# Performance work log

Hardware: AMD Instinct MI355X
Metric: run time of the kernel (lower is better)

The kernel has to match this reference:

```python
import jax, jax.numpy as jnp
import numpy as np

V, E, H = 50000, 512, 1024
HD = H // 2            # per-direction LSTM hidden
T = 2048               # sequence length
TAGS, START, STOP = 32, 30, 31
NEG = -10000.0


def setup_inputs() -> dict:
    key = jax.random.key(0)
    ks = jax.random.split(key, 14)
    s = 1.0 / np.sqrt(HD)
    u = lambda k, shape: jax.random.uniform(k, shape, jnp.float32, -s, s)
    sentence = jax.random.randint(ks[0], (T,), 0, V)
    emb = jax.random.normal(ks[1], (V, E), jnp.float32)
    # PyTorch LSTM gate layout: [i, f, g, o] stacked along dim 0
    w_ih_f, w_hh_f, b_f = u(ks[2], (4 * HD, E)), u(ks[3], (4 * HD, HD)), u(ks[4], (4 * HD,))
    w_ih_b, w_hh_b, b_b = u(ks[5], (4 * HD, E)), u(ks[6], (4 * HD, HD)), u(ks[7], (4 * HD,))
    W_out = u(ks[8], (TAGS, H))
    b_out = u(ks[9], (TAGS,))
    transitions = jax.random.normal(ks[10], (TAGS, TAGS), jnp.float32)
    transitions = transitions.at[START, :].set(NEG).at[:, STOP].set(NEG)
    h0 = jax.random.normal(ks[11], (2, HD), jnp.float32)  # [dir, HD], batch=1 squeezed
    c0 = jax.random.normal(ks[12], (2, HD), jnp.float32)
    return dict(sentence=sentence, emb=emb, w_ih_f=w_ih_f, w_hh_f=w_hh_f, b_f=b_f,
                w_ih_b=w_ih_b, w_hh_b=w_hh_b, b_b=b_b, W_out=W_out, b_out=b_out,
                transitions=transitions, h0=h0, c0=c0)


def _lstm_dir(x, h0, c0, w_ih, w_hh, b, reverse):
    # x: [T, E]; single-sequence LSTM scan, gates ordered i,f,g,o as in torch
    xg = x @ w_ih.T + b  # [T, 4*HD], precompute input contribution
    def step(carry, xt):
        h, c = carry
        g = xt + w_hh @ h
        i, f, gg, o = jnp.split(g, 4)
        c = jax.nn.sigmoid(f) * c + jax.nn.sigmoid(i) * jnp.tanh(gg)
        h = jax.nn.sigmoid(o) * jnp.tanh(c)
        return (h, c), h
    _, hs = jax.lax.scan(step, (h0, c0), xg, reverse=reverse)
    return hs  # [T, HD]


def _viterbi(feats, transitions):
    # feats: [T, TAGS]
    init = jnp.full((TAGS,), NEG, feats.dtype).at[START].set(0.0)
    def step(fv, feat):
        scores = fv[None, :] + transitions       # [next, prev]
        bp = jnp.argmax(scores, axis=1)          # [TAGS]
        fv_new = jnp.max(scores, axis=1) + feat
        return fv_new, bp
    fv, bps = jax.lax.scan(step, init, feats)
    terminal = fv + transitions[STOP]
    best = jnp.argmax(terminal)
    score = terminal[best]
    def back(tag, bp):
        return bp[tag], tag
    _, path = jax.lax.scan(back, best, bps, reverse=True)
    return score, path  # path: [T] int tags


def reference(sentence, emb, w_ih_f, w_hh_f, b_f, w_ih_b, w_hh_b, b_b,
              W_out, b_out, transitions, h0, c0):
    x = emb[sentence]  # [T, E]
    hf = _lstm_dir(x, h0[0], c0[0], w_ih_f, w_hh_f, b_f, reverse=False)
    hb = _lstm_dir(x, h0[1], c0[1], w_ih_b, w_hh_b, b_b, reverse=True)
    feats = jnp.concatenate([hf, hb], axis=-1) @ W_out.T + b_out  # [T, TAGS]
    score, path = _viterbi(feats, transitions)
    return score, path
```

## Files before the change

### kernel.cpp

```cpp
#include <hip/hip_runtime.h>
#include <math.h>

#define TT 2048
#define EE 512
#define HDD 512
#define TAGS 32
#define STARTT 30
#define STOPP 31
#define NEGV -10000.0f
#define VCH 256
#define SENT 0xFFFFFFFFu

__global__ __launch_bounds__(256) void k_xgemm(const int* __restrict__ sent,
        const float* __restrict__ emb,
        const float* __restrict__ wf, const float* __restrict__ wb,
        const float* __restrict__ bf, const float* __restrict__ bb,
        float* __restrict__ xg, int* __restrict__ xflag) {
    const int jj   = blockIdx.y >> 1;
    const int dir  = blockIdx.y & 1;
    const int tile = dir ? (31 - jj) : jj;
    const float* __restrict__ w    = dir ? wb : wf;
    const float* __restrict__ bias = dir ? bb : bf;
    const int tb = tile * 64;
    const int nb = blockIdx.x * 64;
    __shared__ float As[64][17];
    __shared__ float Bs[64][17];
    const int tid = threadIdx.x;
    const int lr = tid >> 2;
    const int lc = (tid & 3) * 4;
    const int ty = tid >> 4;
    const int tx = tid & 15;
    const int sidx = sent[tb + lr];
    float acc[4][4] = {};
    for (int k0 = 0; k0 < EE; k0 += 16) {
        float4 av = *(const float4*)(emb + (size_t)sidx * EE + k0 + lc);
        float4 bv = *(const float4*)(w + (size_t)(nb + lr) * EE + k0 + lc);
        As[lr][lc+0] = av.x; As[lr][lc+1] = av.y; As[lr][lc+2] = av.z; As[lr][lc+3] = av.w;
        Bs[lr][lc+0] = bv.x; Bs[lr][lc+1] = bv.y; Bs[lr][lc+2] = bv.z; Bs[lr][lc+3] = bv.w;
        __syncthreads();
        #pragma unroll
        for (int kk = 0; kk < 16; ++kk) {
            float a[4], b[4];
            #pragma unroll
            for (int i = 0; i < 4; ++i) a[i] = As[ty*4+i][kk];
            #pragma unroll
            for (int j = 0; j < 4; ++j) b[j] = Bs[tx*4+j][kk];
            #pragma unroll
            for (int i = 0; i < 4; ++i)
                #pragma unroll
                for (int j = 0; j < 4; ++j)
                    acc[i][j] += a[i] * b[j];
        }
        __syncthreads();
    }
    #pragma unroll
    for (int i = 0; i < 4; ++i) {
        float4 o;
        o.x = acc[i][0] + bias[nb + tx*4 + 0];
        o.y = acc[i][1] + bias[nb + tx*4 + 1];
        o.z = acc[i][2] + bias[nb + tx*4 + 2];
        o.w = acc[i][3] + bias[nb + tx*4 + 3];
        *(float4*)(xg + ((size_t)dir*TT + tb + ty*4 + i) * 2048 + nb + tx*4) = o;
    }
    __syncthreads();
    if (tid == 0)
        __hip_atomic_fetch_add(&xflag[dir * 32 + tile], 1,
                               __ATOMIC_RELEASE, __HIP_MEMORY_SCOPE_AGENT);
}

__device__ __forceinline__ float fsig(float x) {
    return __builtin_amdgcn_rcpf(1.f + __expf(-x));
}
__device__ __forceinline__ float ftanh(float x) {
    return 2.f * __builtin_amdgcn_rcpf(1.f + __expf(-2.f * x)) - 1.f;
}

__device__ __forceinline__ void waitflag(const int* f) {
    while (__hip_atomic_load(f, __ATOMIC_ACQUIRE, __HIP_MEMORY_SCOPE_AGENT) < 32)
        __builtin_amdgcn_s_sleep(1);
}

__global__ __launch_bounds__(256, 1) void k_lstm(const float* __restrict__ xg,
        const float* __restrict__ whhf, const float* __restrict__ whhb,
        const float* __restrict__ h0, const float* __restrict__ c0,
        float* __restrict__ hs, const int* __restrict__ xflag) {
    const int dir = blockIdx.y;
    const float* __restrict__ whh = dir ? whhb : whhf;
    const int tid    = threadIdx.x;
    const int lane   = tid & 63;
    const int waveid = tid >> 6;
    const int unit   = lane >> 4;
    const int gate   = (lane >> 2) & 3;
    const int seg    = lane & 3;
    const int ubase  = (blockIdx.x * 4 + waveid) * 4;
    const int grow   = gate * HDD + ubase + unit;

    float4 w[32];
    {
        const float4* wp = (const float4*)(whh + (size_t)grow * HDD + seg * 128);
        #pragma unroll
        for (int i = 0; i < 32; ++i) w[i] = wp[i];
    }

    __shared__ float hbuf[2][528];

    float c = c0[dir * HDD + ubase + unit];

    const int* flags = xflag + dir * 32;
    const int t0 = dir ? (TT - 1) : 0;
    int curtile = t0 >> 6;
    waitflag(&flags[curtile]);
    float xvn = __uint_as_float(__hip_atomic_load(
        (const unsigned*)(xg + ((size_t)dir * TT + t0) * 2048 + grow),
        __ATOMIC_RELAXED, __HIP_MEMORY_SCOPE_AGENT));

    const int g0 = 2 * tid;
    const int soff = (g0 >> 7) * 132 + (g0 & 127);
    hbuf[0][soff]     = h0[dir * HDD + g0];
    hbuf[0][soff + 1] = h0[dir * HDD + g0 + 1];

    for (int s = 0; s < TT; ++s) {
        const int t = dir ? (TT - 1 - s) : s;
        const float xv = xvn;
        if (s + 1 < TT) {
            const int tn = dir ? (TT - 2 - s) : (s + 1);
            const int tilen = tn >> 6;
            if (tilen != curtile) { waitflag(&flags[tilen]); curtile = tilen; }
            xvn = __uint_as_float(__hip_atomic_load(
                (const unsigned*)(xg + ((size_t)dir * TT + tn) * 2048 + grow),
                __ATOMIC_RELAXED, __HIP_MEMORY_SCOPE_AGENT));
        }

        float* hb = hbuf[s & 1];
        if (s > 0) {
            const int tprev = dir ? (t + 1) : (t - 1);
            const unsigned long long* hsrc = (const unsigned long long*)
                (hs + ((size_t)dir * TT + tprev) * HDD) + tid;
            unsigned long long vv = __hip_atomic_load(hsrc,
                    __ATOMIC_RELAXED, __HIP_MEMORY_SCOPE_AGENT);
            while ((unsigned)vv == SENT || (unsigned)(vv >> 32) == SENT)
                vv = __hip_atomic_load(hsrc,
                        __ATOMIC_RELAXED, __HIP_MEMORY_SCOPE_AGENT);
            hb[soff]     = __uint_as_float((unsigned)vv);
            hb[soff + 1] = __uint_as_float((unsigned)(vv >> 32));
        }
        __syncthreads();

        const float4* hp = (const float4*)(hb + seg * 132);
        float a0 = 0.f, a1 = 0.f, a2 = 0.f, a3 = 0.f;
        #pragma unroll
        for (int i = 0; i < 32; i += 4) {
            float4 h0v = hp[i], h1v = hp[i+1], h2v = hp[i+2], h3v = hp[i+3];
            a0 += w[i  ].x*h0v.x + w[i  ].y*h0v.y + w[i  ].z*h0v.z + w[i  ].w*h0v.w;
            a1 += w[i+1].x*h1v.x + w[i+1].y*h1v.y + w[i+1].z*h1v.z + w[i+1].w*h1v.w;
            a2 += w[i+2].x*h2v.x + w[i+2].y*h2v.y + w[i+2].z*h2v.z + w[i+2].w*h2v.w;
            a3 += w[i+3].x*h3v.x + w[i+3].y*h3v.y + w[i+3].z*h3v.z + w[i+3].w*h3v.w;
        }
        float acc = (a0 + a1) + (a2 + a3);
        acc += __shfl_xor(acc, 1);
        acc += __shfl_xor(acc, 2);
        acc += xv;

        const int base = lane & ~15;
        const float iv = __shfl(acc, base + 0);
        const float fv = __shfl(acc, base + 4);
        const float gv = __shfl(acc, base + 8);
        const float ov = __shfl(acc, base + 12);
        c = fsig(fv) * c + fsig(iv) * ftanh(gv);
        const float h = fsig(ov) * ftanh(c);

        if ((lane & 15) == 0)
            __hip_atomic_store(&hs[((size_t)dir * TT + t) * HDD + ubase + unit], h,
                               __ATOMIC_RELAXED, __HIP_MEMORY_SCOPE_AGENT);
    }
}

__global__ __launch_bounds__(256) void k_feats(const float* __restrict__ hs,
        const float* __restrict__ Wout, const float* __restrict__ bout,
        float* __restrict__ feats) {
    const int t = blockIdx.x;
    const int tid = threadIdx.x;
    const int tag = tid >> 3;
    const int chunk = tid & 7;
    const float* __restrict__ hrow = (chunk < 4)
        ? hs + (size_t)t * HDD
        : hs + ((size_t)TT + t) * HDD - 512;
    float acc = 0.f;
    const float4* wp = (const float4*)(Wout + (size_t)tag * 1024 + chunk * 128);
    const float4* hp = (const float4*)(hrow + chunk * 128);
    #pragma unroll
    for (int i = 0; i < 32; ++i) {
        float4 wv = wp[i];
        float4 hv = hp[i];
        acc += wv.x*hv.x + wv.y*hv.y + wv.z*hv.z + wv.w*hv.w;
    }
    __shared__ float red[TAGS][9];
    red[tag][chunk] = acc;
    __syncthreads();
    if (tid < TAGS) {
        float s = bout[tid];
        #pragma unroll
        for (int c = 0; c < 8; ++c) s += red[tid][c];
        feats[(size_t)t * TAGS + tid] = s;
    }
}

__global__ __launch_bounds__(64) void k_viterbi(const float* __restrict__ feats,
        const float* __restrict__ trans, float* __restrict__ out) {
    const int lane = threadIdx.x;
    const int n  = lane & 31;
    const int ph = lane >> 5;
    __shared__ float fvs[TAGS];
    __shared__ unsigned char bp[TT][TAGS];
    __shared__ __align__(16) float fbuf[VCH * TAGS];
    float tr[16];
    #pragma unroll
    for (int p = 0; p < 16; ++p) tr[p] = trans[n * TAGS + ph * 16 + p];
    if (lane < TAGS) fvs[lane] = (lane == STARTT) ? 0.f : NEGV;
    __syncthreads();
    for (int c0 = 0; c0 < TT; c0 += VCH) {
        const float4* src = (const float4*)(feats + (size_t)c0 * TAGS);
        float4* dst = (float4*)fbuf;
        for (int i = lane; i < VCH * TAGS / 4; i += 64) dst[i] = src[i];
        __syncthreads();
        for (int lt = 0; lt < VCH; ++lt) {
            const int t = c0 + lt;
            float bv = fvs[ph * 16] + tr[0];
            int bi = ph * 16;
            #pragma unroll
            for (int p = 1; p < 16; ++p) {
                const float cand = fvs[ph * 16 + p] + tr[p];
                if (cand > bv) { bv = cand; bi = ph * 16 + p; }
            }
            const float obv = __shfl_xor(bv, 32);
            const int   obi = __shfl_xor(bi, 32);
            if (obv > bv || (obv == bv && obi < bi)) { bv = obv; bi = obi; }
            const float nf = bv + fbuf[lt * TAGS + n];
            if (ph == 0) bp[t][n] = (unsigned char)bi;
            __syncthreads();
            if (ph == 0) fvs[n] = nf;
            __syncthreads();
        }
    }
    if (lane < TAGS) fvs[lane] += trans[STOPP * TAGS + lane];
    __syncthreads();
    if (lane == 0) {
        float bs = fvs[0]; int best = 0;
        for (int i = 1; i < TAGS; ++i)
            if (fvs[i] > bs) { bs = fvs[i]; best = i; }
        out[0] = bs;
        int tag = best;
        for (int t = TT - 1; t >= 0; --t) {
            out[1 + t] = (float)tag;
            tag = bp[t][tag];
        }
    }
}

extern "C" void kernel_launch(void* const* d_in, const int* in_sizes, int n_in,
                              void* d_out, int out_size, void* d_ws, size_t ws_size,
                              hipStream_t stream) {
    const int*   sent  = (const int*)  d_in[0];
    const float* emb   = (const float*)d_in[1];
    const float* wihf  = (const float*)d_in[2];
    const float* whhf  = (const float*)d_in[3];
    const float* bfv   = (const float*)d_in[4];
    const float* wihb  = (const float*)d_in[5];
    const float* whhb  = (const float*)d_in[6];
    const float* bbv   = (const float*)d_in[7];
    const float* Wout  = (const float*)d_in[8];
    const float* bout  = (const float*)d_in[9];
    const float* trans = (const float*)d_in[10];
    const float* h0    = (const float*)d_in[11];
    const float* c0    = (const float*)d_in[12];
    float* out = (float*)d_out;

    char* ws = (char*)d_ws;
    float* xg    = (float*)(ws + ((size_t)4  << 20));
    float* hs    = (float*)(ws + ((size_t)36 << 20));
    float* feats = (float*)(ws + ((size_t)44 << 20));
    int* xflag   = (int*)  (ws + ((size_t)44 << 20) + (320u << 10));

    hipMemsetAsync(hs, 0xFF, (size_t)2 * TT * HDD * sizeof(float), stream);
    hipMemsetAsync(xflag, 0, 64 * sizeof(int), stream);
    k_xgemm  <<<dim3(32, 64), 256, 0, stream>>>(sent, emb, wihf, wihb, bfv, bbv,
                                                xg, xflag);
    k_lstm   <<<dim3(32, 2), 256, 0, stream>>>(xg, whhf, whhb, h0, c0, hs, xflag);
    k_feats  <<<TT, 256, 0, stream>>>(hs, Wout, bout, feats);
    k_viterbi<<<1, 64, 0, stream>>>(feats, trans, out);
}
```

Before: 4.496 ms.

## Interleave forward and backward LSTM directions within each block to hide sync latency

The LSTM kernel now runs both directions in the same 32 blocks instead of 64 blocks split by direction. Each block holds both recurrent weight slices in registers and alternates a backward step and a forward step, so the cross-block polling for one direction overlaps with compute for the other. This halves the number of blocks participating in each spin-wait and doubles the register footprint (256 floats of weights per thread), which risks spilling or lower clocks. The serial chain per block also becomes twice as long per iteration.

```diff
diff --git a/kernel.cpp b/kernel.cpp
--- a/kernel.cpp
+++ b/kernel.cpp
@@ -84,8 +84,6 @@
         const float* __restrict__ whhf, const float* __restrict__ whhb,
         const float* __restrict__ h0, const float* __restrict__ c0,
         float* __restrict__ hs, const int* __restrict__ xflag) {
-    const int dir = blockIdx.y;
-    const float* __restrict__ whh = dir ? whhb : whhf;
     const int tid    = threadIdx.x;
     const int lane   = tid & 63;
     const int waveid = tid >> 6;
@@ -95,83 +93,134 @@
     const int ubase  = (blockIdx.x * 4 + waveid) * 4;
     const int grow   = gate * HDD + ubase + unit;
 
-    float4 w[32];
+    float4 wF[32], wB[32];
     {
-        const float4* wp = (const float4*)(whh + (size_t)grow * HDD + seg * 128);
+        const float4* wp = (const float4*)(whhf + (size_t)grow * HDD + seg * 128);
         #pragma unroll
-        for (int i = 0; i < 32; ++i) w[i] = wp[i];
-    }
-
-    __shared__ float hbuf[2][528];
-
-    float c = c0[dir * HDD + ubase + unit];
-
-    const int* flags = xflag + dir * 32;
-    const int t0 = dir ? (TT - 1) : 0;
-    int curtile = t0 >> 6;
-    waitflag(&flags[curtile]);
-    float xvn = __uint_as_float(__hip_atomic_load(
-        (const unsigned*)(xg + ((size_t)dir * TT + t0) * 2048 + grow),
-        __ATOMIC_RELAXED, __HIP_MEMORY_SCOPE_AGENT));
+        for (int i = 0; i < 32; ++i) wF[i] = wp[i];
+        const float4* wq = (const float4*)(whhb + (size_t)grow * HDD + seg * 128);
+        #pragma unroll
+        for (int i = 0; i < 32; ++i) wB[i] = wq[i];
+    }
+
+    __shared__ float hbF[528];
+    __shared__ float hbB[528];
+
+    float cF = c0[ubase + unit];
+    float cB = c0[HDD + ubase + unit];
 
     const int g0 = 2 * tid;
     const int soff = (g0 >> 7) * 132 + (g0 & 127);
-    hbuf[0][soff]     = h0[dir * HDD + g0];
-    hbuf[0][soff + 1] = h0[dir * HDD + g0 + 1];
+    hbF[soff]     = h0[g0];
+    hbF[soff + 1] = h0[g0 + 1];
+    hbB[soff]     = h0[HDD + g0];
+    hbB[soff + 1] = h0[HDD + g0 + 1];
+
+    const int* flagsF = xflag;
+    const int* flagsB = xflag + 32;
+    int ctF = 0, ctB = 31;
+    waitflag(&flagsF[0]);
+    waitflag(&flagsB[31]);
+    float xvF = __uint_as_float(__hip_atomic_load(
+        (const unsigned*)(xg + (size_t)0 * 2048 + grow),
+        __ATOMIC_RELAXED, __HIP_MEMORY_SCOPE_AGENT));
+    float xvB = __uint_as_float(__hip_atomic_load(
+        (const unsigned*)(xg + ((size_t)TT + TT - 1) * 2048 + grow),
+        __ATOMIC_RELAXED, __HIP_MEMORY_SCOPE_AGENT));
 
     for (int s = 0; s < TT; ++s) {
-        const int t = dir ? (TT - 1 - s) : s;
-        const float xv = xvn;
+        const int tf = s;
+        const int tb = TT - 1 - s;
+        const float xf = xvF, xb = xvB;
         if (s + 1 < TT) {
-            const int tn = dir ? (TT - 2 - s) : (s + 1);
-            const int tilen = tn >> 6;
-            if (tilen != curtile) { waitflag(&flags[tilen]); curtile = tilen; }
-            xvn = __uint_as_float(__hip_atomic_load(
-                (const unsigned*)(xg + ((size_t)dir * TT + tn) * 2048 + grow),
+            const int tfn = s + 1, tbn = TT - 2 - s;
+            if ((tfn >> 6) != ctF) { waitflag(&flagsF[tfn >> 6]); ctF = tfn >> 6; }
+            if ((tbn >> 6) != ctB) { waitflag(&flagsB[tbn >> 6]); ctB = tbn >> 6; }
+            xvF = __uint_as_float(__hip_atomic_load(
+                (const unsigned*)(xg + (size_t)tfn * 2048 + grow),
                 __ATOMIC_RELAXED, __HIP_MEMORY_SCOPE_AGENT));
-        }
-
-        float* hb = hbuf[s & 1];
+            xvB = __uint_as_float(__hip_atomic_load(
+                (const unsigned*)(xg + ((size_t)TT + tbn) * 2048 + grow),
+                __ATOMIC_RELAXED, __HIP_MEMORY_SCOPE_AGENT));
+        }
+
         if (s > 0) {
-            const int tprev = dir ? (t + 1) : (t - 1);
             const unsigned long long* hsrc = (const unsigned long long*)
-                (hs + ((size_t)dir * TT + tprev) * HDD) + tid;
+                (hs + ((size_t)TT + tb + 1) * HDD) + tid;
             unsigned long long vv = __hip_atomic_load(hsrc,
                     __ATOMIC_RELAXED, __HIP_MEMORY_SCOPE_AGENT);
             while ((unsigned)vv == SENT || (unsigned)(vv >> 32) == SENT)
                 vv = __hip_atomic_load(hsrc,
                         __ATOMIC_RELAXED, __HIP_MEMORY_SCOPE_AGENT);
-            hb[soff]     = __uint_as_float((unsigned)vv);
-            hb[soff + 1] = __uint_as_float((unsigned)(vv >> 32));
-        }
-        __syncthreads();
-
-        const float4* hp = (const float4*)(hb + seg * 132);
-        float a0 = 0.f, a1 = 0.f, a2 = 0.f, a3 = 0.f;
-        #pragma unroll
-        for (int i = 0; i < 32; i += 4) {
-            float4 h0v = hp[i], h1v = hp[i+1], h2v = hp[i+2], h3v = hp[i+3];
-            a0 += w[i  ].x*h0v.x + w[i  ].y*h0v.y + w[i  ].z*h0v.z + w[i  ].w*h0v.w;
-            a1 += w[i+1].x*h1v.x + w[i+1].y*h1v.y + w[i+1].z*h1v.z + w[i+1].w*h1v.w;
-            a2 += w[i+2].x*h2v.x + w[i+2].y*h2v.y + w[i+2].z*h2v.z + w[i+2].w*h2v.w;
-            a3 += w[i+3].x*h3v.x + w[i+3].y*h3v.y + w[i+3].z*h3v.z + w[i+3].w*h3v.w;
-        }
-        float acc = (a0 + a1) + (a2 + a3);
-        acc += __shfl_xor(acc, 1);
-        acc += __shfl_xor(acc, 2);
-        acc += xv;
-
-        const int base = lane & ~15;
-        const float iv = __shfl(acc, base + 0);
-        const float fv = __shfl(acc, base + 4);
-        const float gv = __shfl(acc, base + 8);
-        const float ov = __shfl(acc, base + 12);
-        c = fsig(fv) * c + fsig(iv) * ftanh(gv);
-        const float h = fsig(ov) * ftanh(c);
-
-        if ((lane & 15) == 0)
-            __hip_atomic_store(&hs[((size_t)dir * TT + t) * HDD + ubase + unit], h,
-                               __ATOMIC_RELAXED, __HIP_MEMORY_SCOPE_AGENT);
+            hbB[soff]     = __uint_as_float((unsigned)vv);
+            hbB[soff + 1] = __uint_as_float((unsigned)(vv >> 32));
+        }
+        __syncthreads();
+        {
+            const float4* hp = (const float4*)(hbB + seg * 132);
+            float a0 = 0.f, a1 = 0.f, a2 = 0.f, a3 = 0.f;
+            #pragma unroll
+            for (int i = 0; i < 32; i += 4) {
+                float4 h0v = hp[i], h1v = hp[i+1], h2v = hp[i+2], h3v = hp[i+3];
+                a0 += wB[i  ].x*h0v.x + wB[i  ].y*h0v.y + wB[i  ].z*h0v.z + wB[i  ].w*h0v.w;
+                a1 += wB[i+1].x*h1v.x + wB[i+1].y*h1v.y + wB[i+1].z*h1v.z + wB[i+1].w*h1v.w;
+                a2 += wB[i+2].x*h2v.x + wB[i+2].y*h2v.y + wB[i+2].z*h2v.z + wB[i+2].w*h2v.w;
+                a3 += wB[i+3].x*h3v.x + wB[i+3].y*h3v.y + wB[i+3].z*h3v.z + wB[i+3].w*h3v.w;
+            }
+            float acc = (a0 + a1) + (a2 + a3);
+            acc += __shfl_xor(acc, 1);
+            acc += __shfl_xor(acc, 2);
+            acc += xb;
+            const int base = lane & ~15;
+            const float iv = __shfl(acc, base + 0);
+            const float fv = __shfl(acc, base + 4);
+            const float gv = __shfl(acc, base + 8);
+            const float ov = __shfl(acc, base + 12);
+            cB = fsig(fv) * cB + fsig(iv) * ftanh(gv);
+            const float h = fsig(ov) * ftanh(cB);
+            if ((lane & 15) == 0)
+                __hip_atomic_store(&hs[((size_t)TT + tb) * HDD + ubase + unit], h,
+                                   __ATOMIC_RELAXED, __HIP_MEMORY_SCOPE_AGENT);
+        }
+
+        if (s > 0) {
+            const unsigned long long* hsrc = (const unsigned long long*)
+                (hs + (size_t)(tf - 1) * HDD) + tid;
+            unsigned long long vv = __hip_atomic_load(hsrc,
+                    __ATOMIC_RELAXED, __HIP_MEMORY_SCOPE_AGENT);
+            while ((unsigned)vv == SENT || (unsigned)(vv >> 32) == SENT)
+                vv = __hip_atomic_load(hsrc,
+                        __ATOMIC_RELAXED, __HIP_MEMORY_SCOPE_AGENT);
+            hbF[soff]     = __uint_as_float((unsigned)vv);
+            hbF[soff + 1] = __uint_as_float((unsigned)(vv >> 32));
+        }
+        __syncthreads();
+        {
+            const float4* hp = (const float4*)(hbF + seg * 132);
+            float a0 = 0.f, a1 = 0.f, a2 = 0.f, a3 = 0.f;
+            #pragma unroll
+            for (int i = 0; i < 32; i += 4) {
+                float4 h0v = hp[i], h1v = hp[i+1], h2v = hp[i+2], h3v = hp[i+3];
+                a0 += wF[i  ].x*h0v.x + wF[i  ].y*h0v.y + wF[i  ].z*h0v.z + wF[i  ].w*h0v.w;
+                a1 += wF[i+1].x*h1v.x + wF[i+1].y*h1v.y + wF[i+1].z*h1v.z + wF[i+1].w*h1v.w;
+                a2 += wF[i+2].x*h2v.x + wF[i+2].y*h2v.y + wF[i+2].z*h2v.z + wF[i+2].w*h2v.w;
+                a3 += wF[i+3].x*h3v.x + wF[i+3].y*h3v.y + wF[i+3].z*h3v.z + wF[i+3].w*h3v.w;
+            }
+            float acc = (a0 + a1) + (a2 + a3);
+            acc += __shfl_xor(acc, 1);
+            acc += __shfl_xor(acc, 2);
+            acc += xf;
+            const int base = lane & ~15;
+            const float iv = __shfl(acc, base + 0);
+            const float fv = __shfl(acc, base + 4);
+            const float gv = __shfl(acc, base + 8);
+            const float ov = __shfl(acc, base + 12);
+            cF = fsig(fv) * cF + fsig(iv) * ftanh(gv);
+            const float h = fsig(ov) * ftanh(cF);
+            if ((lane & 15) == 0)
+                __hip_atomic_store(&hs[(size_t)tf * HDD + ubase + unit], h,
+                                   __ATOMIC_RELAXED, __HIP_MEMORY_SCOPE_AGENT);
+        }
     }
 }
 
@@ -285,7 +334,7 @@
     hipMemsetAsync(xflag, 0, 64 * sizeof(int), stream);
     k_xgemm  <<<dim3(32, 64), 256, 0, stream>>>(sent, emb, wihf, wihb, bfv, bbv,
                                                 xg, xflag);
-    k_lstm   <<<dim3(32, 2), 256, 0, stream>>>(xg, whhf, whhb, h0, c0, hs, xflag);
+    k_lstm   <<<dim3(32), 256, 0, stream>>>(xg, whhf, whhb, h0, c0, hs, xflag);
     k_feats  <<<TT, 256, 0, stream>>>(hs, Wout, bout, feats);
     k_viterbi<<<1, 64, 0, stream>>>(feats, trans, out);
 }
```

Result: slower. 6.933 ms (+54.2%).

## Fuse input GEMM and LSTM recurrence into one kernel to overlap via flags

Applied to the files above, without the earlier changes.

Merges the input-projection GEMM and the recurrent LSTM kernel into a single launch. The first 64 blocks run the recurrence and the remaining 2048 blocks compute xg tiles and signal per-tile flags. The recurrence can therefore start while the GEMM is still running, rather than waiting for a separate kernel boundary. This relies on the 64 LSTM blocks being scheduled first and co-resident. Launch bounds change to allow 2 blocks per CU, which may limit the LSTM's register-resident weights.

```diff
diff --git a/kernel.cpp b/kernel.cpp
--- a/kernel.cpp
+++ b/kernel.cpp
@@ -11,88 +11,92 @@
 #define VCH 256
 #define SENT 0xFFFFFFFFu
 
-__global__ __launch_bounds__(256) void k_xgemm(const int* __restrict__ sent,
-        const float* __restrict__ emb,
-        const float* __restrict__ wf, const float* __restrict__ wb,
-        const float* __restrict__ bf, const float* __restrict__ bb,
-        float* __restrict__ xg, int* __restrict__ xflag) {
-    const int jj   = blockIdx.y >> 1;
-    const int dir  = blockIdx.y & 1;
-    const int tile = dir ? (31 - jj) : jj;
-    const float* __restrict__ w    = dir ? wb : wf;
-    const float* __restrict__ bias = dir ? bb : bf;
-    const int tb = tile * 64;
-    const int nb = blockIdx.x * 64;
-    __shared__ float As[64][17];
-    __shared__ float Bs[64][17];
-    const int tid = threadIdx.x;
-    const int lr = tid >> 2;
-    const int lc = (tid & 3) * 4;
-    const int ty = tid >> 4;
-    const int tx = tid & 15;
-    const int sidx = sent[tb + lr];
-    float acc[4][4] = {};
-    for (int k0 = 0; k0 < EE; k0 += 16) {
-        float4 av = *(const float4*)(emb + (size_t)sidx * EE + k0 + lc);
-        float4 bv = *(const float4*)(w + (size_t)(nb + lr) * EE + k0 + lc);
-        As[lr][lc+0] = av.x; As[lr][lc+1] = av.y; As[lr][lc+2] = av.z; As[lr][lc+3] = av.w;
-        Bs[lr][lc+0] = bv.x; Bs[lr][lc+1] = bv.y; Bs[lr][lc+2] = bv.z; Bs[lr][lc+3] = bv.w;
-        __syncthreads();
-        #pragma unroll
-        for (int kk = 0; kk < 16; ++kk) {
-            float a[4], b[4];
-            #pragma unroll
-            for (int i = 0; i < 4; ++i) a[i] = As[ty*4+i][kk];
-            #pragma unroll
-            for (int j = 0; j < 4; ++j) b[j] = Bs[tx*4+j][kk];
-            #pragma unroll
-            for (int i = 0; i < 4; ++i)
-                #pragma unroll
-                for (int j = 0; j < 4; ++j)
-                    acc[i][j] += a[i] * b[j];
-        }
-        __syncthreads();
-    }
-    #pragma unroll
-    for (int i = 0; i < 4; ++i) {
-        float4 o;
-        o.x = acc[i][0] + bias[nb + tx*4 + 0];
-        o.y = acc[i][1] + bias[nb + tx*4 + 1];
-        o.z = acc[i][2] + bias[nb + tx*4 + 2];
-        o.w = acc[i][3] + bias[nb + tx*4 + 3];
-        *(float4*)(xg + ((size_t)dir*TT + tb + ty*4 + i) * 2048 + nb + tx*4) = o;
-    }
-    __syncthreads();
-    if (tid == 0)
-        __hip_atomic_fetch_add(&xflag[dir * 32 + tile], 1,
-                               __ATOMIC_RELEASE, __HIP_MEMORY_SCOPE_AGENT);
-}
-
 __device__ __forceinline__ float fsig(float x) {
     return __builtin_amdgcn_rcpf(1.f + __expf(-x));
 }
 __device__ __forceinline__ float ftanh(float x) {
     return 2.f * __builtin_amdgcn_rcpf(1.f + __expf(-2.f * x)) - 1.f;
 }
-
 __device__ __forceinline__ void waitflag(const int* f) {
     while (__hip_atomic_load(f, __ATOMIC_ACQUIRE, __HIP_MEMORY_SCOPE_AGENT) < 32)
         __builtin_amdgcn_s_sleep(1);
 }
 
-__global__ __launch_bounds__(256, 1) void k_lstm(const float* __restrict__ xg,
-        const float* __restrict__ whhf, const float* __restrict__ whhb,
+__global__ __launch_bounds__(256, 2) void k_main(
+        const int* __restrict__ sent, const float* __restrict__ emb,
+        const float* __restrict__ wihf, const float* __restrict__ whhf,
+        const float* __restrict__ bfv,
+        const float* __restrict__ wihb, const float* __restrict__ whhb,
+        const float* __restrict__ bbv,
         const float* __restrict__ h0, const float* __restrict__ c0,
-        float* __restrict__ hs, const int* __restrict__ xflag) {
-    const int dir = blockIdx.y;
+        float* __restrict__ xg, float* __restrict__ hs,
+        int* __restrict__ xflag) {
+    const int tid = threadIdx.x;
+
+    if (blockIdx.x >= 64) {
+        const int gid  = blockIdx.x - 64;
+        const int gy   = gid >> 5;
+        const int jj   = gy >> 1;
+        const int dir  = gy & 1;
+        const int tile = dir ? (31 - jj) : jj;
+        const float* __restrict__ w    = dir ? wihb : wihf;
+        const float* __restrict__ bias = dir ? bbv : bfv;
+        const int tb = tile * 64;
+        const int nb = (gid & 31) * 64;
+        __shared__ float As[64][17];
+        __shared__ float Bs[64][17];
+        const int lr = tid >> 2;
+        const int lc = (tid & 3) * 4;
+        const int ty = tid >> 4;
+        const int tx = tid & 15;
+        const int sidx = sent[tb + lr];
+        float acc[4][4] = {};
+        for (int k0 = 0; k0 < EE; k0 += 16) {
+            float4 av = *(const float4*)(emb + (size_t)sidx * EE + k0 + lc);
+            float4 bv = *(const float4*)(w + (size_t)(nb + lr) * EE + k0 + lc);
+            As[lr][lc+0] = av.x; As[lr][lc+1] = av.y; As[lr][lc+2] = av.z; As[lr][lc+3] = av.w;
+            Bs[lr][lc+0] = bv.x; Bs[lr][lc+1] = bv.y; Bs[lr][lc+2] = bv.z; Bs[lr][lc+3] = bv.w;
+            __syncthreads();
+            #pragma unroll
+            for (int kk = 0; kk < 16; ++kk) {
+                float a[4], b[4];
+                #pragma unroll
+                for (int i = 0; i < 4; ++i) a[i] = As[ty*4+i][kk];
+                #pragma unroll
+                for (int j = 0; j < 4; ++j) b[j] = Bs[tx*4+j][kk];
+                #pragma unroll
+                for (int i = 0; i < 4; ++i)
+                    #pragma unroll
+                    for (int j = 0; j < 4; ++j)
+                        acc[i][j] += a[i] * b[j];
+            }
+            __syncthreads();
+        }
+        #pragma unroll
+        for (int i = 0; i < 4; ++i) {
+            float4 o;
+            o.x = acc[i][0] + bias[nb + tx*4 + 0];
+            o.y = acc[i][1] + bias[nb + tx*4 + 1];
+            o.z = acc[i][2] + bias[nb + tx*4 + 2];
+            o.w = acc[i][3] + bias[nb + tx*4 + 3];
+            *(float4*)(xg + ((size_t)dir*TT + tb + ty*4 + i) * 2048 + nb + tx*4) = o;
+        }
+        __syncthreads();
+        if (tid == 0)
+            __hip_atomic_fetch_add(&xflag[dir * 32 + tile], 1,
+                                   __ATOMIC_RELEASE, __HIP_MEMORY_SCOPE_AGENT);
+        return;
+    }
+
+    const int wg  = blockIdx.x & 31;
+    const int dir = blockIdx.x >> 5;
     const float* __restrict__ whh = dir ? whhb : whhf;
-    const int tid    = threadIdx.x;
     const int lane   = tid & 63;
     const int waveid = tid >> 6;
     const int unit   = lane >> 4;
     const int gate   = (lane >> 2) & 3;
     const int seg    = lane & 3;
-    const int ubase  = (blockIdx.x * 4 + waveid) * 4;
+    const int ubase  = (wg * 4 + waveid) * 4;
     const int grow   = gate * HDD + ubase + unit;
 
     float4 w[32];
@@ -283,9 +287,9 @@
 
     hipMemsetAsync(hs, 0xFF, (size_t)2 * TT * HDD * sizeof(float), stream);
     hipMemsetAsync(xflag, 0, 64 * sizeof(int), stream);
-    k_xgemm  <<<dim3(32, 64), 256, 0, stream>>>(sent, emb, wihf, wihb, bfv, bbv,
-                                                xg, xflag);
-    k_lstm   <<<dim3(32, 2), 256, 0, stream>>>(xg, whhf, whhb, h0, c0, hs, xflag);
+    k_main   <<<dim3(64 + 2048), 256, 0, stream>>>(sent, emb, wihf, whhf, bfv,
+                                                   wihb, whhb, bbv, h0, c0,
+                                                   xg, hs, xflag);
     k_feats  <<<TT, 256, 0, stream>>>(hs, Wout, bout, feats);
     k_viterbi<<<1, 64, 0, stream>>>(feats, trans, out);
 }
```

After: 4.446 ms. About the same (-1.1%).
